# Optimization experiments

Hardware: AMD Instinct MI355X
Metric: run time of the kernel (lower is better)

Reference implementation:

```python
import jax, jax.numpy as jnp
import numpy as np

B, T, N, F_IN = 32, 64, 128, 16
H, SOUT = 64, 16
D = N * SOUT            # transformer d_model = 2048
NHEADS, DH = 16, 128
DFF, LAYERS = 2048, 2
NCLASSES, OUT = 8, 10
THR = 0.004             # edge threshold on sigmoid(V)/N


def setup_inputs():
    key = jax.random.key(0)
    ks = iter(jax.random.split(key, 40))
    r = lambda *s: jax.random.normal(next(ks), s, jnp.float32) * 0.02
    return {
        'X': jax.random.normal(next(ks), (B, T, N * F_IN), jnp.float32),
        'V_Adap': jax.random.normal(next(ks), (NCLASSES, N, N), jnp.float32),
        'Wl': r(F_IN, H), 'bl': jnp.zeros((H,)),
        'Wr': r(F_IN, H), 'br': jnp.zeros((H,)),
        'att': jax.random.normal(next(ks), (H,), jnp.float32) * 0.1,
        'gat_bias': jnp.zeros((H,)),
        'Wfc': r(H, SOUT), 'bfc': jnp.zeros((SOUT,)),
        'Wq': r(LAYERS, D, D), 'bq': jnp.zeros((LAYERS, D)),
        'Wk': r(LAYERS, D, D), 'bk': jnp.zeros((LAYERS, D)),
        'Wv': r(LAYERS, D, D), 'bv': jnp.zeros((LAYERS, D)),
        'Wo': r(LAYERS, D, D), 'bo': jnp.zeros((LAYERS, D)),
        'ln1_g': jnp.ones((LAYERS, D)), 'ln1_b': jnp.zeros((LAYERS, D)),
        'W1': r(LAYERS, D, DFF), 'b1': jnp.zeros((LAYERS, DFF)),
        'W2': r(LAYERS, DFF, D), 'b2': jnp.zeros((LAYERS, D)),
        'ln2_g': jnp.ones((LAYERS, D)), 'ln2_b': jnp.zeros((LAYERS, D)),
        'Wout': r(D, OUT), 'bout': jnp.zeros((OUT,)),
        'class_idx': 2,
    }


def _ln(x, g, b):
    mu = jnp.mean(x, -1, keepdims=True)
    var = jnp.var(x, -1, keepdims=True)
    return (x - mu) / jnp.sqrt(var + 1e-5) * g + b


def reference(X, V_Adap, Wl, bl, Wr, br, att, gat_bias, Wfc, bfc,
              Wq, bq, Wk, bk, Wv, bv, Wo, bo, ln1_g, ln1_b,
              W1, b1, W2, b2, ln2_g, ln2_b, Wout, bout, class_idx):
    # dynamic adjacency: sigmoid + scale + threshold (data-dependent sparsity as a mask)
    A = jax.nn.sigmoid(V_Adap[class_idx]) / N
    mask = (A > THR) | jnp.eye(N, dtype=bool)   # GATv2Conv default add_self_loops

    def gat_step(x_t):                           # x_t: (B, N, F_IN)
        xl = x_t @ Wl + bl                       # source transform (B, N, H)
        xr = x_t @ Wr + br                       # target transform (B, N, H)
        s = jax.nn.leaky_relu(xl[:, :, None, :] + xr[:, None, :, :], 0.2)  # (B, src, dst, H)
        e = jnp.where(mask[None], jnp.einsum('bijh,h->bij', s, att), -1e9)
        alpha = jax.nn.softmax(e, axis=1)        # softmax over sources per target node
        out = jnp.einsum('bij,bih->bjh', alpha, xl) + gat_bias
        return out @ Wfc + bfc                   # (B, N, SOUT)

    Xr = X.reshape(B, T, N, F_IN).transpose(1, 0, 2, 3)   # (T, B, N, F)
    spatial = jax.lax.map(gat_step, Xr)                   # (T, B, N, SOUT)
    h = spatial.transpose(1, 0, 2, 3).reshape(B, T, D)

    # post-norm TransformerEncoder (torch defaults: relu, d_ff=2048, no dropout at eval)
    for l in range(LAYERS):
        q = (h @ Wq[l] + bq[l]).reshape(B, T, NHEADS, DH).transpose(0, 2, 1, 3)
        k = (h @ Wk[l] + bk[l]).reshape(B, T, NHEADS, DH).transpose(0, 2, 1, 3)
        v = (h @ Wv[l] + bv[l]).reshape(B, T, NHEADS, DH).transpose(0, 2, 1, 3)
        aw = jax.nn.softmax(jnp.einsum('bhqd,bhkd->bhqk', q, k) / np.float32(np.sqrt(DH)), axis=-1)
        ao = jnp.einsum('bhqk,bhkd->bhqd', aw, v).transpose(0, 2, 1, 3).reshape(B, T, D)
        h = _ln(h + ao @ Wo[l] + bo[l], ln1_g[l], ln1_b[l])
        ff = jax.nn.relu(h @ W1[l] + b1[l]) @ W2[l] + b2[l]
        h = _ln(h + ff, ln2_g[l], ln2_b[l])

    return h[:, -1, :] @ Wout + bout             # (B, OUT)
```

## Files before the change

### kernel.cpp

```cpp
#include <hip/hip_runtime.h>
#include <cstdint>
#include <cstddef>


typedef unsigned short u16;
typedef __bf16 bf16x8 __attribute__((ext_vector_type(8)));
typedef float f32x4 __attribute__((ext_vector_type(4)));
typedef unsigned int u32x4 __attribute__((ext_vector_type(4)));
typedef float f32x4v __attribute__((ext_vector_type(4)));

__device__ __forceinline__ u16 f2b(float f) {
  union { float f; unsigned u; } x; x.f = f;
  unsigned r = x.u + 0x7fffu + ((x.u >> 16) & 1u);
  return (u16)(r >> 16);
}
__device__ __forceinline__ float b2f(u16 s) {
  union { unsigned u; float f; } x; x.u = ((unsigned)s) << 16;
  return x.f;
}

__device__ __forceinline__ void gload_lds16(const void* g, void* l) {
  __builtin_amdgcn_global_load_lds(
      (const __attribute__((address_space(1))) unsigned int*)g,
      (__attribute__((address_space(3))) unsigned int*)l, 16, 0, 0);
}

__global__ __launch_bounds__(1024) void gat_kernel(
    const float* __restrict__ X, const float* __restrict__ V_Adap,
    const int* __restrict__ class_idx,
    const float* __restrict__ Wl, const float* __restrict__ bl,
    const float* __restrict__ Wr, const float* __restrict__ br,
    const float* __restrict__ att, const float* __restrict__ gat_bias,
    const float* __restrict__ Wfc, const float* __restrict__ bfc,
    float* __restrict__ h_f32, u16* __restrict__ h_b16)
{
  const int bt = blockIdx.x;
  const int tid = threadIdx.x;

  __shared__ __align__(16) float xlT[64 * 132];
  __shared__ __align__(16) float xrT[64 * 132];
  __shared__ __align__(16) float xln[128 * 68];
  __shared__ __align__(16) u16   esb[128 * 128];
  __shared__ __align__(16) float WlT[64 * 20];
  __shared__ __align__(16) float WrT[64 * 20];
  __shared__ __align__(16) float Wfcs[64 * 16];
  __shared__ float atts[64], bls[64], brs[64], gbias[64], bfcs[16];
  __shared__ float cls[128], crs[128], inv_s[128];
  __shared__ float red[8 * 128];

  if (tid < 1024) {
    const int h = tid >> 4, f = tid & 15;
    WlT[h * 20 + f] = Wl[f * 64 + h];
    WrT[h * 20 + f] = Wr[f * 64 + h];
    Wfcs[tid] = Wfc[tid];
  }
  if (tid < 64) { atts[tid] = att[tid]; bls[tid] = bl[tid]; brs[tid] = br[tid]; gbias[tid] = gat_bias[tid]; }
  if (tid < 16) bfcs[tid] = bfc[tid];
  const int cidx = *class_idx;
  __syncthreads();

  {
    const int n = tid >> 3, hq = tid & 7;
    const float* xp = X + (size_t)bt * 2048 + n * 16;
    float xv[16];
    #pragma unroll
    for (int f4 = 0; f4 < 4; f4++) {
      f32x4v t4 = ((const f32x4v*)xp)[f4];
      xv[f4 * 4 + 0] = t4[0]; xv[f4 * 4 + 1] = t4[1];
      xv[f4 * 4 + 2] = t4[2]; xv[f4 * 4 + 3] = t4[3];
    }
    #pragma unroll
    for (int k = 0; k < 8; k++) {
      const int h = hq + 8 * k;
      float al = bls[h], ar = brs[h];
      #pragma unroll
      for (int f4 = 0; f4 < 4; f4++) {
        f32x4v wl = *(const f32x4v*)&WlT[h * 20 + f4 * 4];
        f32x4v wr = *(const f32x4v*)&WrT[h * 20 + f4 * 4];
        #pragma unroll
        for (int f = 0; f < 4; f++) {
          al = fmaf(xv[f4 * 4 + f], wl[f], al);
          ar = fmaf(xv[f4 * 4 + f], wr[f], ar);
        }
      }
      xlT[h * 132 + n] = al;
      xrT[h * 132 + n] = ar;
      xln[n * 68 + h] = al;
    }
  }
  __syncthreads();

  if (tid < 256) {
    const int n = tid & 127;
    const float* srcT = (tid < 128) ? xlT : xrT;
    float s = 0.f;
    for (int h = 0; h < 64; h++) s = fmaf(atts[h], srcT[h * 132 + n], s);
    if (tid < 128) cls[n] = s; else crs[n] = s;
  }
  __syncthreads();

  {
    const int i0 = (tid >> 5) * 4;
    const int j0 = tid & 31;
    float acc[4][4] = {};
    #pragma unroll 2
    for (int h = 0; h < 64; h++) {
      const float ah = atts[h];
      f32x4v xa = *(const f32x4v*)&xlT[h * 132 + i0];
      float xb[4];
      #pragma unroll
      for (int b = 0; b < 4; b++) xb[b] = xrT[h * 132 + j0 + 32 * b];
      #pragma unroll
      for (int a = 0; a < 4; a++)
        #pragma unroll
        for (int b = 0; b < 4; b++)
          acc[a][b] = fmaf(ah, __builtin_fabsf(xa[a] + xb[b]), acc[a][b]);
    }
    const float* Vc = V_Adap + (size_t)cidx * 16384;
    #pragma unroll
    for (int a = 0; a < 4; a++) {
      const int i = i0 + a;
      const float ei = 0.6f * cls[i];
      #pragma unroll
      for (int b = 0; b < 4; b++) {
        const int j = j0 + 32 * b;
        const float e = ei + 0.6f * crs[j] + 0.4f * acc[a][b];
        const bool m = (Vc[i * 128 + j] > 0.04800922f) || (i == j);
        esb[i * 128 + j] = f2b(m ? e : -1e9f);
      }
    }
  }
  __syncthreads();

  {
    const int j = tid & 127, c = tid >> 7;
    float ps = 0.f;
    for (int i = c * 16; i < c * 16 + 16; i++) {
      const float p = __expf(b2f(esb[i * 128 + j]));
      esb[i * 128 + j] = f2b(p);
      ps += p;
    }
    red[c * 128 + j] = ps;
  }
  __syncthreads();
  if (tid < 128) {
    float s = 0.f;
    #pragma unroll
    for (int c = 0; c < 8; c++) s += red[c * 128 + tid];
    inv_s[tid] = 1.f / s;
  }
  __syncthreads();

  {
    const int j = tid >> 3, h0 = (tid & 7) * 8;
    float acc[8] = {};
    for (int i = 0; i < 128; i++) {
      const float p = b2f(esb[i * 128 + j]);
      f32x4v x0 = *(const f32x4v*)&xln[i * 68 + h0];
      f32x4v x1 = *(const f32x4v*)&xln[i * 68 + h0 + 4];
      #pragma unroll
      for (int c = 0; c < 4; c++) {
        acc[c] = fmaf(p, x0[c], acc[c]);
        acc[c + 4] = fmaf(p, x1[c], acc[c + 4]);
      }
    }
    const float sc = inv_s[j];
    float* aggb = xlT;
    #pragma unroll
    for (int c = 0; c < 8; c++) aggb[j * 66 + h0 + c] = acc[c] * sc;
  }
  __syncthreads();

  {
    const int j = tid >> 3, s0 = (tid & 7) * 2;
    const float* aggb = xlT;
    float o0 = bfcs[s0], o1 = bfcs[s0 + 1];
    for (int h = 0; h < 64; h++) {
      const float av = aggb[j * 66 + h] + gbias[h];
      o0 = fmaf(av, Wfcs[h * 16 + s0], o0);
      o1 = fmaf(av, Wfcs[h * 16 + s0 + 1], o1);
    }
    const size_t off = (size_t)bt * 2048 + j * 16 + s0;
    h_f32[off] = o0; h_f32[off + 1] = o1;
    h_b16[off] = f2b(o0); h_b16[off + 1] = f2b(o1);
  }
}

struct TransArgs {
  const float* s0; const float* s1; const float* s2;
  u16* d0; u16* d1; u16* d2;
};

__global__ __launch_bounds__(256) void transpose_cast(TransArgs p)
{
  const float* src = (blockIdx.z == 0) ? p.s0 : (blockIdx.z == 1) ? p.s1 : p.s2;
  u16* dst = (blockIdx.z == 0) ? p.d0 : (blockIdx.z == 1) ? p.d1 : p.d2;
  __shared__ u16 tile[64][66];
  const int k0 = blockIdx.y * 64, n0 = blockIdx.x * 64;
  const int tid = threadIdx.x;
  const int c = tid & 63, rb = tid >> 6;
  #pragma unroll
  for (int r = 0; r < 16; r++) {
    const int k = rb + r * 4;
    tile[k][c] = f2b(src[(size_t)(k0 + k) * 2048 + n0 + c]);
  }
  __syncthreads();
  #pragma unroll
  for (int r = 0; r < 16; r++) {
    const int n = rb + r * 4;
    dst[(size_t)(n0 + n) * 2048 + k0 + c] = tile[c][n];
  }
}

struct GemmArgs {
  const u16* A;
  const u16* Bt0; const u16* Bt1; const u16* Bt2;
  const float* b0; const float* b1; const float* b2;
  void* C0; void* C1; void* C2;
  int N; int K;
};

template <int MODE>
__global__ __launch_bounds__(256) void gemm_bt(GemmArgs g)
{
  const int z = blockIdx.z;
  const u16* Bt = (z == 0) ? g.Bt0 : (z == 1) ? g.Bt1 : g.Bt2;
  const float* bias = (z == 0) ? g.b0 : (z == 1) ? g.b1 : g.b2;
  void* C = (z == 0) ? g.C0 : (z == 1) ? g.C1 : g.C2;
  const int N = g.N, K = g.K;
  const int m0 = blockIdx.y * 128, n0 = blockIdx.x * 128;

  __shared__ __align__(16) u16 As[128 * 32];
  __shared__ __align__(16) u16 Bs[128 * 32];

  const int tid = threadIdx.x;
  const int lane = tid & 63, w = tid >> 6;
  const int srow = w * 16 + (lane >> 2);
  const int scol = (lane & 3) * 8;
  const u16* gA = g.A + (size_t)(m0 + srow) * K + scol;
  const u16* gB = Bt + (size_t)(n0 + srow) * K + scol;
  u16* lA0 = &As[(w * 16) * 32];
  u16* lA1 = &As[(64 + w * 16) * 32];
  u16* lB0 = &Bs[(w * 16) * 32];
  u16* lB1 = &Bs[(64 + w * 16) * 32];

  const int wm = (w >> 1) * 64, wn = (w & 1) * 64;
  const int lq = lane >> 4, lr = lane & 15;

  f32x4 acc[4][4] = {};

  for (int k0 = 0; k0 < K; k0 += 32) {
    gload_lds16(gA + k0, lA0);
    gload_lds16(gA + (size_t)64 * K + k0, lA1);
    gload_lds16(gB + k0, lB0);
    gload_lds16(gB + (size_t)64 * K + k0, lB1);
    __syncthreads();

    bf16x8 af[4], bf[4];
    #pragma unroll
    for (int i = 0; i < 4; i++) {
      af[i] = __builtin_bit_cast(bf16x8, *(const u32x4*)&As[(wm + i * 16 + lr) * 32 + lq * 8]);
      bf[i] = __builtin_bit_cast(bf16x8, *(const u32x4*)&Bs[(wn + i * 16 + lr) * 32 + lq * 8]);
    }
    #pragma unroll
    for (int mi = 0; mi < 4; mi++)
      #pragma unroll
      for (int ni = 0; ni < 4; ni++)
        acc[mi][ni] = __builtin_amdgcn_mfma_f32_16x16x32_bf16(af[mi], bf[ni], acc[mi][ni], 0, 0, 0);
    __syncthreads();
  }

  #pragma unroll
  for (int ni = 0; ni < 4; ni++) {
    const int col = n0 + wn + ni * 16 + lr;
    const float bv = bias[col];
    #pragma unroll
    for (int mi = 0; mi < 4; mi++) {
      #pragma unroll
      for (int r = 0; r < 4; r++) {
        const int row = m0 + wm + mi * 16 + lq * 4 + r;
        float v = acc[mi][ni][r] + bv;
        if (MODE == 0) {
          ((float*)C)[(size_t)row * N + col] = v;
        } else {
          if (MODE == 2) v = fmaxf(v, 0.f);
          ((u16*)C)[(size_t)row * N + col] = f2b(v);
        }
      }
    }
  }
}

template <int MODE>
__global__ __launch_bounds__(256) void gemm_bt64(GemmArgs g)
{
  const u16* Bt = g.Bt0;
  const float* bias = g.b0;
  void* C = g.C0;
  const int N = g.N, K = g.K;
  const int m0 = blockIdx.y * 128, n0 = blockIdx.x * 64;

  __shared__ __align__(16) u16 As[128 * 32];
  __shared__ __align__(16) u16 Bs[64 * 32];

  const int tid = threadIdx.x;
  const int lane = tid & 63, w = tid >> 6;
  const int srow = w * 16 + (lane >> 2);
  const int scol = (lane & 3) * 8;
  const u16* gA = g.A + (size_t)(m0 + srow) * K + scol;
  const u16* gB = Bt + (size_t)(n0 + srow) * K + scol;
  u16* lA0 = &As[(w * 16) * 32];
  u16* lA1 = &As[(64 + w * 16) * 32];
  u16* lB0 = &Bs[(w * 16) * 32];

  const int wm = w * 32;
  const int lq = lane >> 4, lr = lane & 15;

  f32x4 acc[2][4] = {};

  for (int k0 = 0; k0 < K; k0 += 32) {
    gload_lds16(gA + k0, lA0);
    gload_lds16(gA + (size_t)64 * K + k0, lA1);
    gload_lds16(gB + k0, lB0);
    __syncthreads();

    bf16x8 af[2], bf[4];
    #pragma unroll
    for (int i = 0; i < 2; i++)
      af[i] = __builtin_bit_cast(bf16x8, *(const u32x4*)&As[(wm + i * 16 + lr) * 32 + lq * 8]);
    #pragma unroll
    for (int i = 0; i < 4; i++)
      bf[i] = __builtin_bit_cast(bf16x8, *(const u32x4*)&Bs[(i * 16 + lr) * 32 + lq * 8]);
    #pragma unroll
    for (int mi = 0; mi < 2; mi++)
      #pragma unroll
      for (int ni = 0; ni < 4; ni++)
        acc[mi][ni] = __builtin_amdgcn_mfma_f32_16x16x32_bf16(af[mi], bf[ni], acc[mi][ni], 0, 0, 0);
    __syncthreads();
  }

  #pragma unroll
  for (int ni = 0; ni < 4; ni++) {
    const int col = n0 + ni * 16 + lr;
    const float bv = bias[col];
    #pragma unroll
    for (int mi = 0; mi < 2; mi++) {
      #pragma unroll
      for (int r = 0; r < 4; r++) {
        const int row = m0 + wm + mi * 16 + lq * 4 + r;
        float v = acc[mi][ni][r] + bv;
        if (MODE == 0) {
          ((float*)C)[(size_t)row * N + col] = v;
        } else {
          if (MODE == 2) v = fmaxf(v, 0.f);
          ((u16*)C)[(size_t)row * N + col] = f2b(v);
        }
      }
    }
  }
}

__global__ __launch_bounds__(256) void attn_kernel(
    const u16* __restrict__ Qb, const u16* __restrict__ Kb,
    const u16* __restrict__ Vb, u16* __restrict__ AOb)
{
  const int head = blockIdx.x, b = blockIdx.y;
  const int tid = threadIdx.x;
  __shared__ __align__(16) float qs[64 * 129];
  __shared__ __align__(16) float ks[64 * 129];
  __shared__ __align__(16) float vs[64 * 128];
  __shared__ __align__(16) float ss[64 * 65];
  const size_t base = ((size_t)b * 64) * 2048 + (size_t)head * 128;

  for (int idx = tid; idx < 8192; idx += 256) {
    const int t_ = idx >> 7, d = idx & 127;
    const size_t gp = base + (size_t)t_ * 2048 + d;
    qs[t_ * 129 + d] = b2f(Qb[gp]);
    ks[t_ * 129 + d] = b2f(Kb[gp]);
    vs[t_ * 128 + d] = b2f(Vb[gp]);
  }
  __syncthreads();

  {
    const int i0 = (tid >> 4) * 4, j0 = (tid & 15) * 4;
    float acc[4][4] = {};
    for (int d = 0; d < 128; d++) {
      float qv[4], kv[4];
      #pragma unroll
      for (int a = 0; a < 4; a++) qv[a] = qs[(i0 + a) * 129 + d];
      #pragma unroll
      for (int c = 0; c < 4; c++) kv[c] = ks[(j0 + c) * 129 + d];
      #pragma unroll
      for (int a = 0; a < 4; a++)
        #pragma unroll
        for (int c = 0; c < 4; c++)
          acc[a][c] = fmaf(qv[a], kv[c], acc[a][c]);
    }
    const float sc = 0.08838834764831845f;
    #pragma unroll
    for (int a = 0; a < 4; a++)
      #pragma unroll
      for (int c = 0; c < 4; c++)
        ss[(i0 + a) * 65 + j0 + c] = acc[a][c] * sc;
  }
  __syncthreads();

  if (tid < 64) {
    float mx = -3e38f;
    for (int j = 0; j < 64; j++) mx = fmaxf(mx, ss[tid * 65 + j]);
    float s = 0.f;
    for (int j = 0; j < 64; j++) {
      const float p = __expf(ss[tid * 65 + j] - mx);
      ss[tid * 65 + j] = p; s += p;
    }
    const float inv = 1.f / s;
    for (int j = 0; j < 64; j++) ss[tid * 65 + j] *= inv;
  }
  __syncthreads();

  {
    const int i0 = (tid >> 4) * 4, d0 = (tid & 15) * 8;
    float o[4][8] = {};
    for (int j = 0; j < 64; j++) {
      float pv[4];
      #pragma unroll
      for (int a = 0; a < 4; a++) pv[a] = ss[(i0 + a) * 65 + j];
      f32x4v v0 = *(const f32x4v*)&vs[j * 128 + d0];
      f32x4v v1 = *(const f32x4v*)&vs[j * 128 + d0 + 4];
      float vv[8] = {v0[0], v0[1], v0[2], v0[3], v1[0], v1[1], v1[2], v1[3]};
      #pragma unroll
      for (int a = 0; a < 4; a++)
        #pragma unroll
        for (int c = 0; c < 8; c++)
          o[a][c] = fmaf(pv[a], vv[c], o[a][c]);
    }
    #pragma unroll
    for (int a = 0; a < 4; a++)
      #pragma unroll
      for (int c = 0; c < 8; c++)
        AOb[base + (size_t)(i0 + a) * 2048 + d0 + c] = f2b(o[a][c]);
  }
}

__global__ __launch_bounds__(256) void ln_kernel(
    const float* __restrict__ hin, const float* __restrict__ delta,
    const float* __restrict__ gamma, const float* __restrict__ beta,
    float* __restrict__ hout, u16* __restrict__ bout_)
{
  const int token = blockIdx.x, tid = threadIdx.x;
  const size_t off = (size_t)token * 2048;
  __shared__ float red[8];
  float v[8];
  float s = 0.f;
  #pragma unroll
  for (int r = 0; r < 8; r++) {
    const int i = r * 256 + tid;
    v[r] = hin[off + i] + delta[off + i];
    s += v[r];
  }
  #pragma unroll
  for (int o = 32; o > 0; o >>= 1) s += __shfl_down(s, o, 64);
  if ((tid & 63) == 0) red[tid >> 6] = s;
  __syncthreads();
  const float mean = (red[0] + red[1] + red[2] + red[3]) * (1.f / 2048.f);
  float s2 = 0.f;
  #pragma unroll
  for (int r = 0; r < 8; r++) { const float d = v[r] - mean; s2 = fmaf(d, d, s2); }
  #pragma unroll
  for (int o = 32; o > 0; o >>= 1) s2 += __shfl_down(s2, o, 64);
  if ((tid & 63) == 0) red[4 + (tid >> 6)] = s2;
  __syncthreads();
  const float var = (red[4] + red[5] + red[6] + red[7]) * (1.f / 2048.f);
  const float rstd = rsqrtf(var + 1e-5f);
  #pragma unroll
  for (int r = 0; r < 8; r++) {
    const int i = r * 256 + tid;
    const float y = (v[r] - mean) * rstd * gamma[i] + beta[i];
    hout[off + i] = y;
    bout_[off + i] = f2b(y);
  }
}

__global__ __launch_bounds__(256) void final_kernel(
    const float* __restrict__ h, const float* __restrict__ Wout,
    const float* __restrict__ bout, float* __restrict__ out)
{
  const int b = blockIdx.x, tid = threadIdx.x;
  __shared__ float row[2048];
  __shared__ float part[256];
  const float* hr = h + ((size_t)b * 64 + 63) * 2048;
  for (int i = tid; i < 2048; i += 256) row[i] = hr[i];
  __syncthreads();
  const int o = tid & 15, ch = tid >> 4;
  float s = 0.f;
  if (o < 10) {
    const int i0 = ch * 128;
    for (int i = i0; i < i0 + 128; i++) s = fmaf(row[i], Wout[(size_t)i * 10 + o], s);
  }
  part[tid] = s;
  __syncthreads();
  if (tid < 10) {
    float t = bout[tid];
    for (int c2 = 0; c2 < 16; c2++) t += part[c2 * 16 + tid];
    out[(size_t)b * 10 + tid] = t;
  }
}

extern "C" void kernel_launch(void* const* d_in, const int* in_sizes, int n_in,
                              void* d_out, int out_size, void* d_ws, size_t ws_size,
                              hipStream_t stream)
{
  const float* X        = (const float*)d_in[0];
  const float* V_Adap   = (const float*)d_in[1];
  const float* Wl       = (const float*)d_in[2];
  const float* bl       = (const float*)d_in[3];
  const float* Wr       = (const float*)d_in[4];
  const float* br       = (const float*)d_in[5];
  const float* att      = (const float*)d_in[6];
  const float* gat_bias = (const float*)d_in[7];
  const float* Wfc      = (const float*)d_in[8];
  const float* bfc      = (const float*)d_in[9];
  const float* Wq       = (const float*)d_in[10];
  const float* bq       = (const float*)d_in[11];
  const float* Wk       = (const float*)d_in[12];
  const float* bk       = (const float*)d_in[13];
  const float* Wv       = (const float*)d_in[14];
  const float* bv       = (const float*)d_in[15];
  const float* Wo       = (const float*)d_in[16];
  const float* bo       = (const float*)d_in[17];
  const float* ln1_g    = (const float*)d_in[18];
  const float* ln1_b    = (const float*)d_in[19];
  const float* W1       = (const float*)d_in[20];
  const float* b1       = (const float*)d_in[21];
  const float* W2       = (const float*)d_in[22];
  const float* b2       = (const float*)d_in[23];
  const float* ln2_g    = (const float*)d_in[24];
  const float* ln2_b    = (const float*)d_in[25];
  const float* WoutP    = (const float*)d_in[26];
  const float* boutP    = (const float*)d_in[27];
  const int*   class_idx = (const int*)d_in[28];

  char* ws = (char*)d_ws;
  const size_t MB = (size_t)1 << 20;
  float* h_f32 = (float*)(ws);
  u16*   h_b16 = (u16*)(ws + 16 * MB);
  u16*   Qb    = (u16*)(ws + 24 * MB);
  u16*   Kb    = (u16*)(ws + 32 * MB);
  u16*   Vb    = (u16*)(ws + 40 * MB);
  u16*   AOb   = (u16*)(ws + 48 * MB);
  float* tmp   = (float*)(ws + 56 * MB);
  u16*   ff1b  = (u16*)(ws + 72 * MB);
  u16*   Wt0   = (u16*)(ws + 80 * MB);
  u16*   Wt1   = (u16*)(ws + 88 * MB);
  u16*   Wt2   = (u16*)(ws + 96 * MB);

  gat_kernel<<<2048, 1024, 0, stream>>>(X, V_Adap, class_idx, Wl, bl, Wr, br,
                                        att, gat_bias, Wfc, bfc, h_f32, h_b16);

  const size_t DD = 2048ull * 2048ull;
  for (int l = 0; l < 2; l++) {
    const size_t wofs = (size_t)l * DD;
    const size_t bofs = (size_t)l * 2048;

    transpose_cast<<<dim3(32, 32, 3), 256, 0, stream>>>(
        TransArgs{Wq + wofs, Wk + wofs, Wv + wofs, Wt0, Wt1, Wt2});
    gemm_bt<1><<<dim3(16, 16, 3), 256, 0, stream>>>(
        GemmArgs{h_b16, Wt0, Wt1, Wt2, bq + bofs, bk + bofs, bv + bofs,
                 Qb, Kb, Vb, 2048, 2048});

    attn_kernel<<<dim3(16, 32), 256, 0, stream>>>(Qb, Kb, Vb, AOb);

    transpose_cast<<<dim3(32, 32, 1), 256, 0, stream>>>(
        TransArgs{Wo + wofs, nullptr, nullptr, Wt0, nullptr, nullptr});
    gemm_bt64<0><<<dim3(32, 16), 256, 0, stream>>>(
        GemmArgs{AOb, Wt0, nullptr, nullptr, bo + bofs, nullptr, nullptr,
                 tmp, nullptr, nullptr, 2048, 2048});
    ln_kernel<<<2048, 256, 0, stream>>>(h_f32, tmp, ln1_g + bofs, ln1_b + bofs,
                                        h_f32, h_b16);

    transpose_cast<<<dim3(32, 32, 1), 256, 0, stream>>>(
        TransArgs{W1 + wofs, nullptr, nullptr, Wt0, nullptr, nullptr});
    gemm_bt64<2><<<dim3(32, 16), 256, 0, stream>>>(
        GemmArgs{h_b16, Wt0, nullptr, nullptr, b1 + bofs, nullptr, nullptr,
                 ff1b, nullptr, nullptr, 2048, 2048});

    transpose_cast<<<dim3(32, 32, 1), 256, 0, stream>>>(
        TransArgs{W2 + wofs, nullptr, nullptr, Wt0, nullptr, nullptr});
    gemm_bt64<0><<<dim3(32, 16), 256, 0, stream>>>(
        GemmArgs{ff1b, Wt0, nullptr, nullptr, b2 + bofs, nullptr, nullptr,
                 tmp, nullptr, nullptr, 2048, 2048});
    ln_kernel<<<2048, 256, 0, stream>>>(h_f32, tmp, ln2_g + bofs, ln2_b + bofs,
                                        h_f32, h_b16);
  }

  final_kernel<<<32, 256, 0, stream>>>(h_f32, WoutP, boutP, (float*)d_out);
}
```

Before: 1.067 ms.

## Use MFMA for GAT aggregation, transpose score layout, batch weight transposes

```diff
diff --git a/kernel.cpp b/kernel.cpp
--- a/kernel.cpp
+++ b/kernel.cpp
@@ -8,6 +8,7 @@
 typedef float f32x4 __attribute__((ext_vector_type(4)));
 typedef unsigned int u32x4 __attribute__((ext_vector_type(4)));
 typedef float f32x4v __attribute__((ext_vector_type(4)));
+typedef unsigned short u16x4 __attribute__((ext_vector_type(4)));
 
 __device__ __forceinline__ u16 f2b(float f) {
   union { float f; unsigned u; } x; x.f = f;
@@ -16,6 +17,14 @@
 }
 __device__ __forceinline__ float b2f(u16 s) {
   union { unsigned u; float f; } x; x.u = ((unsigned)s) << 16;
+  return x.f;
+}
+__device__ __forceinline__ float b2f_lo(unsigned q) {
+  union { unsigned u; float f; } x; x.u = q << 16;
+  return x.f;
+}
+__device__ __forceinline__ float b2f_hi(unsigned q) {
+  union { unsigned u; float f; } x; x.u = q & 0xffff0000u;
   return x.f;
 }
 
@@ -39,20 +48,21 @@
 
   __shared__ __align__(16) float xlT[64 * 132];
   __shared__ __align__(16) float xrT[64 * 132];
-  __shared__ __align__(16) float xln[128 * 68];
-  __shared__ __align__(16) u16   esb[128 * 128];
+  __shared__ __align__(16) u16   xlTb[64 * 136];
+  __shared__ __align__(16) u16   esbT[128 * 136];
+  __shared__ __align__(16) u16   aggb[128 * 72];
   __shared__ __align__(16) float WlT[64 * 20];
   __shared__ __align__(16) float WrT[64 * 20];
-  __shared__ __align__(16) float Wfcs[64 * 16];
+  __shared__ __align__(16) float WfcT[16 * 66];
   __shared__ float atts[64], bls[64], brs[64], gbias[64], bfcs[16];
   __shared__ float cls[128], crs[128], inv_s[128];
   __shared__ float red[8 * 128];
 
-  if (tid < 1024) {
+  {
     const int h = tid >> 4, f = tid & 15;
     WlT[h * 20 + f] = Wl[f * 64 + h];
     WrT[h * 20 + f] = Wr[f * 64 + h];
-    Wfcs[tid] = Wfc[tid];
+    WfcT[f * 66 + h] = Wfc[h * 16 + f];
   }
   if (tid < 64) { atts[tid] = att[tid]; bls[tid] = bl[tid]; brs[tid] = br[tid]; gbias[tid] = gat_bias[tid]; }
   if (tid < 16) bfcs[tid] = bfc[tid];
@@ -85,7 +95,7 @@
       }
       xlT[h * 132 + n] = al;
       xrT[h * 132 + n] = ar;
-      xln[n * 68 + h] = al;
+      xlTb[h * 136 + n] = f2b(al);
     }
   }
   __syncthreads();
@@ -101,15 +111,13 @@
 
   {
     const int i0 = (tid >> 5) * 4;
-    const int j0 = tid & 31;
+    const int j0 = (tid & 31) * 4;
     float acc[4][4] = {};
     #pragma unroll 2
     for (int h = 0; h < 64; h++) {
       const float ah = atts[h];
       f32x4v xa = *(const f32x4v*)&xlT[h * 132 + i0];
-      float xb[4];
-      #pragma unroll
-      for (int b = 0; b < 4; b++) xb[b] = xrT[h * 132 + j0 + 32 * b];
+      f32x4v xb = *(const f32x4v*)&xrT[h * 132 + j0];
       #pragma unroll
       for (int a = 0; a < 4; a++)
         #pragma unroll
@@ -117,28 +125,45 @@
           acc[a][b] = fmaf(ah, __builtin_fabsf(xa[a] + xb[b]), acc[a][b]);
     }
     const float* Vc = V_Adap + (size_t)cidx * 16384;
+    float vm[4][4];
     #pragma unroll
     for (int a = 0; a < 4; a++) {
-      const int i = i0 + a;
-      const float ei = 0.6f * cls[i];
-      #pragma unroll
-      for (int b = 0; b < 4; b++) {
-        const int j = j0 + 32 * b;
-        const float e = ei + 0.6f * crs[j] + 0.4f * acc[a][b];
-        const bool m = (Vc[i * 128 + j] > 0.04800922f) || (i == j);
-        esb[i * 128 + j] = f2b(m ? e : -1e9f);
-      }
-    }
-  }
-  __syncthreads();
-
-  {
-    const int j = tid & 127, c = tid >> 7;
+      f32x4v vc = *(const f32x4v*)&Vc[(size_t)(i0 + a) * 128 + j0];
+      #pragma unroll
+      for (int b = 0; b < 4; b++) vm[a][b] = vc[b];
+    }
+    #pragma unroll
+    for (int b = 0; b < 4; b++) {
+      const int j = j0 + b;
+      const float ej = 0.6f * crs[j];
+      u16x4 pk;
+      #pragma unroll
+      for (int a = 0; a < 4; a++) {
+        const int i = i0 + a;
+        const float e = ej + 0.6f * cls[i] + 0.4f * acc[a][b];
+        const bool m = (vm[a][b] > 0.04800922f) || (i == j);
+        pk[a] = f2b(m ? e : -1e9f);
+      }
+      *(u16x4*)&esbT[j * 136 + i0] = pk;
+    }
+  }
+  __syncthreads();
+
+  {
+    const int j = tid >> 3, c = tid & 7;
+    u16* rp = &esbT[j * 136 + c * 16];
     float ps = 0.f;
-    for (int i = c * 16; i < c * 16 + 16; i++) {
-      const float p = __expf(b2f(esb[i * 128 + j]));
-      esb[i * 128 + j] = f2b(p);
-      ps += p;
+    #pragma unroll
+    for (int half = 0; half < 2; half++) {
+      u32x4 q = *(u32x4*)(rp + half * 8);
+      #pragma unroll
+      for (int w2 = 0; w2 < 4; w2++) {
+        const float p0 = __expf(b2f_lo(q[w2]));
+        const float p1 = __expf(b2f_hi(q[w2]));
+        ps += p0 + p1;
+        q[w2] = (unsigned)f2b(p0) | ((unsigned)f2b(p1) << 16);
+      }
+      *(u32x4*)(rp + half * 8) = q;
     }
     red[c * 128 + j] = ps;
   }
@@ -152,33 +177,50 @@
   __syncthreads();
 
   {
-    const int j = tid >> 3, h0 = (tid & 7) * 8;
-    float acc[8] = {};
-    for (int i = 0; i < 128; i++) {
-      const float p = b2f(esb[i * 128 + j]);
-      f32x4v x0 = *(const f32x4v*)&xln[i * 68 + h0];
-      f32x4v x1 = *(const f32x4v*)&xln[i * 68 + h0 + 4];
-      #pragma unroll
-      for (int c = 0; c < 4; c++) {
-        acc[c] = fmaf(p, x0[c], acc[c]);
-        acc[c + 4] = fmaf(p, x1[c], acc[c + 4]);
-      }
-    }
-    const float sc = inv_s[j];
-    float* aggb = xlT;
-    #pragma unroll
-    for (int c = 0; c < 8; c++) aggb[j * 66 + h0 + c] = acc[c] * sc;
+    const int w = tid >> 6, lane = tid & 63;
+    const int lq = lane >> 4, lr = lane & 15;
+    const int jt = w >> 1, ht0 = (w & 1) * 2;
+    f32x4 acc2[2] = {};
+    #pragma unroll
+    for (int ks = 0; ks < 4; ks++) {
+      const bf16x8 af = __builtin_bit_cast(bf16x8,
+          *(const u32x4*)&esbT[(jt * 16 + lr) * 136 + ks * 32 + lq * 8]);
+      #pragma unroll
+      for (int t = 0; t < 2; t++) {
+        const bf16x8 bfb = __builtin_bit_cast(bf16x8,
+            *(const u32x4*)&xlTb[((ht0 + t) * 16 + lr) * 136 + ks * 32 + lq * 8]);
+        acc2[t] = __builtin_amdgcn_mfma_f32_16x16x32_bf16(af, bfb, acc2[t], 0, 0, 0);
+      }
+    }
+    #pragma unroll
+    for (int t = 0; t < 2; t++) {
+      const int h = (ht0 + t) * 16 + lr;
+      const float gb = gbias[h];
+      #pragma unroll
+      for (int r = 0; r < 4; r++) {
+        const int j = jt * 16 + lq * 4 + r;
+        aggb[j * 72 + h] = f2b(acc2[t][r] * inv_s[j] + gb);
+      }
+    }
   }
   __syncthreads();
 
   {
     const int j = tid >> 3, s0 = (tid & 7) * 2;
-    const float* aggb = xlT;
     float o0 = bfcs[s0], o1 = bfcs[s0 + 1];
-    for (int h = 0; h < 64; h++) {
-      const float av = aggb[j * 66 + h] + gbias[h];
-      o0 = fmaf(av, Wfcs[h * 16 + s0], o0);
-      o1 = fmaf(av, Wfcs[h * 16 + s0 + 1], o1);
+    #pragma unroll
+    for (int h8 = 0; h8 < 8; h8++) {
+      u32x4 q = *(const u32x4*)&aggb[j * 72 + h8 * 8];
+      #pragma unroll
+      for (int w2 = 0; w2 < 4; w2++) {
+        const int h = h8 * 8 + w2 * 2;
+        const float a0 = b2f_lo(q[w2]);
+        const float a1 = b2f_hi(q[w2]);
+        o0 = fmaf(a0, WfcT[s0 * 66 + h], o0);
+        o1 = fmaf(a0, WfcT[(s0 + 1) * 66 + h], o1);
+        o0 = fmaf(a1, WfcT[s0 * 66 + h + 1], o0);
+        o1 = fmaf(a1, WfcT[(s0 + 1) * 66 + h + 1], o1);
+      }
     }
     const size_t off = (size_t)bt * 2048 + j * 16 + s0;
     h_f32[off] = o0; h_f32[off + 1] = o1;
@@ -570,24 +612,21 @@
 
     attn_kernel<<<dim3(16, 32), 256, 0, stream>>>(Qb, Kb, Vb, AOb);
 
-    transpose_cast<<<dim3(32, 32, 1), 256, 0, stream>>>(
-        TransArgs{Wo + wofs, nullptr, nullptr, Wt0, nullptr, nullptr});
+    transpose_cast<<<dim3(32, 32, 3), 256, 0, stream>>>(
+        TransArgs{Wo + wofs, W1 + wofs, W2 + wofs, Wt0, Wt1, Wt2});
+
     gemm_bt64<0><<<dim3(32, 16), 256, 0, stream>>>(
         GemmArgs{AOb, Wt0, nullptr, nullptr, bo + bofs, nullptr, nullptr,
                  tmp, nullptr, nullptr, 2048, 2048});
     ln_kernel<<<2048, 256, 0, stream>>>(h_f32, tmp, ln1_g + bofs, ln1_b + bofs,
                                         h_f32, h_b16);
 
-    transpose_cast<<<dim3(32, 32, 1), 256, 0, stream>>>(
-        TransArgs{W1 + wofs, nullptr, nullptr, Wt0, nullptr, nullptr});
     gemm_bt64<2><<<dim3(32, 16), 256, 0, stream>>>(
-        GemmArgs{h_b16, Wt0, nullptr, nullptr, b1 + bofs, nullptr, nullptr,
+        GemmArgs{h_b16, Wt1, nullptr, nullptr, b1 + bofs, nullptr, nullptr,
                  ff1b, nullptr, nullptr, 2048, 2048});
 
-    transpose_cast<<<dim3(32, 32, 1), 256, 0, stream>>>(
-        TransArgs{W2 + wofs, nullptr, nullptr, Wt0, nullptr, nullptr});
     gemm_bt64<0><<<dim3(32, 16), 256, 0, stream>>>(
-        GemmArgs{ff1b, Wt0, nullptr, nullptr, b2 + bofs, nullptr, nullptr,
+        GemmArgs{ff1b, Wt2, nullptr, nullptr, b2 + bofs, nullptr, nullptr,
                  tmp, nullptr, nullptr, 2048, 2048});
     ln_kernel<<<2048, 256, 0, stream>>>(h_f32, tmp, ln2_g + bofs, ln2_b + bofs,
                                         h_f32, h_b16);
```

After: 966.5 us. 1.1x faster.
